# Optimization experiments

Hardware: AMD Instinct MI355X
Metric: run time of the kernel (lower is better)

## Reference

```python
import jax, jax.numpy as jnp
import numpy as np

N_NODES = 100000
N_EDGES = 3200000
D_IN = 16
D_OUT = 32


def setup_inputs() -> dict:
    key = jax.random.key(0)
    ks = jax.random.split(key, 8)
    x = jax.random.normal(ks[0], (N_NODES, D_IN), dtype=jnp.float32)
    edge_index = jax.random.randint(ks[1], (2, N_EDGES), 0, N_NODES, dtype=jnp.int64)
    s = 1.0 / np.sqrt(D_IN)
    # mlp1: Linear(16,16) -> ReLU -> Linear(16,16)
    w1 = jax.random.uniform(ks[2], (D_IN, D_IN), jnp.float32, -s, s)
    b1 = jax.random.uniform(ks[3], (D_IN,), jnp.float32, -s, s)
    w2 = jax.random.uniform(ks[4], (D_IN, D_IN), jnp.float32, -s, s)
    b2 = jax.random.uniform(ks[5], (D_IN,), jnp.float32, -s, s)
    # SAGEConv(16,32): lin_l (neighbors, with bias), lin_r (root, no bias)
    wl = jax.random.uniform(ks[6], (D_IN, D_OUT), jnp.float32, -s, s)
    bl = jnp.zeros((D_OUT,), jnp.float32)
    wr = jax.random.uniform(ks[7], (D_IN, D_OUT), jnp.float32, -s, s)
    return {"x": x, "edge_index": edge_index, "w1": w1, "b1": b1,
            "w2": w2, "b2": b2, "wl": wl, "bl": bl, "wr": wr}


def reference(x, edge_index, w1, b1, w2, b2, wl, bl, wr):
    # MLP: Linear -> ReLU -> Linear
    h = jax.nn.relu(x @ w1 + b1) @ w2 + b2  # [N, 16]
    src, dst = edge_index[0], edge_index[1]
    # mean aggregation of neighbor (source) features at destination nodes
    msg = h[src]  # [E, 16]
    summed = jax.ops.segment_sum(msg, dst, num_segments=N_NODES)  # [N, 16]
    cnt = jax.ops.segment_sum(jnp.ones((msg.shape[0],), h.dtype), dst,
                              num_segments=N_NODES)
    mean = summed / jnp.maximum(cnt, 1.0)[:, None]
    # SAGEConv: lin_l(aggr) + lin_r(root)
    out = mean @ wl + bl + h @ wr  # [N, 32]
    return out
```

## Files before the change

kernel.cpp:

```cpp
#include <hip/hip_runtime.h>
#include <hip/hip_bf16.h>

#define D_IN_C 16
#define BUCKET_SHIFT 9
#define BUCKET_NODES 512
#define CAP 18432
#define PT 16
#define PART_CHUNK 4096

__global__ __launch_bounds__(256) void mlp_kernel(
    const float* __restrict__ x,
    const float* __restrict__ w1, const float* __restrict__ b1,
    const float* __restrict__ w2, const float* __restrict__ b2,
    float* __restrict__ h, int* __restrict__ bcur,
    int n_nodes) {
  __shared__ float sw1[256];
  __shared__ float sw2[256];
  __shared__ float sb1[16];
  __shared__ float sb2[16];
  int t = threadIdx.x;
  if (blockIdx.x == 0) bcur[t] = 0;
  sw1[t] = w1[t];
  sw2[t] = w2[t];
  if (t < 16) { sb1[t] = b1[t]; sb2[t] = b2[t]; }
  __syncthreads();

  int n = blockIdx.x * blockDim.x + t;
  if (n >= n_nodes) return;

  float xi[16];
  const float4* xr = (const float4*)(x + (size_t)n * 16);
  float4 v0 = xr[0], v1 = xr[1], v2 = xr[2], v3 = xr[3];
  xi[0]=v0.x; xi[1]=v0.y; xi[2]=v0.z; xi[3]=v0.w;
  xi[4]=v1.x; xi[5]=v1.y; xi[6]=v1.z; xi[7]=v1.w;
  xi[8]=v2.x; xi[9]=v2.y; xi[10]=v2.z; xi[11]=v2.w;
  xi[12]=v3.x; xi[13]=v3.y; xi[14]=v3.z; xi[15]=v3.w;

  float t1[16];
#pragma unroll
  for (int j = 0; j < 16; ++j) {
    float acc = sb1[j];
#pragma unroll
    for (int k = 0; k < 16; ++k) acc += xi[k] * sw1[k * 16 + j];
    t1[j] = fmaxf(acc, 0.0f);
  }
  float hh[16];
#pragma unroll
  for (int j = 0; j < 16; ++j) {
    float acc = sb2[j];
#pragma unroll
    for (int k = 0; k < 16; ++k) acc += t1[k] * sw2[k * 16 + j];
    hh[j] = acc;
  }

  float4* hw = (float4*)(h + (size_t)n * 16);
  hw[0] = make_float4(hh[0], hh[1], hh[2], hh[3]);
  hw[1] = make_float4(hh[4], hh[5], hh[6], hh[7]);
  hw[2] = make_float4(hh[8], hh[9], hh[10], hh[11]);
  hw[3] = make_float4(hh[12], hh[13], hh[14], hh[15]);
}

__global__ __launch_bounds__(256) void part_kernel(
    const int* __restrict__ src, const int* __restrict__ dst,
    int* __restrict__ bcur, int* __restrict__ part,
    int* __restrict__ cnt, int nbuck, int n_edges) {
  __shared__ int lhist[256];
  __shared__ int lofs[256];
  int t = threadIdx.x;
  int base = blockIdx.x * PART_CHUNK;

  int zi = blockIdx.x * 256 + t;
  if (zi < nbuck * BUCKET_NODES) cnt[zi] = 0;

  if (t < nbuck) lhist[t] = 0;
  __syncthreads();

  int d[PT], s[PT];
#pragma unroll
  for (int i = 0; i < PT; ++i) {
    int e = base + i * 256 + t;
    if (e < n_edges) { d[i] = dst[e]; s[i] = src[e]; }
    else d[i] = -1;
  }
#pragma unroll
  for (int i = 0; i < PT; ++i) {
    if (d[i] >= 0) atomicAdd(&lhist[d[i] >> BUCKET_SHIFT], 1);
  }
  __syncthreads();
  if (t < nbuck) {
    int c = lhist[t];
    int r = (c > 0) ? atomicAdd(&bcur[t], c) : 0;
    lofs[t] = t * CAP + r;
  }
  __syncthreads();
#pragma unroll
  for (int i = 0; i < PT; ++i) {
    if (d[i] >= 0) {
      int b = d[i] >> BUCKET_SHIFT;
      int p = atomicAdd(&lofs[b], 1);
      part[p] = ((d[i] & (BUCKET_NODES - 1)) << 17) | s[i];
    }
  }
}

__global__ __launch_bounds__(256) void acc_kernel(
    const float* __restrict__ h, const int* __restrict__ part,
    const int* __restrict__ bcur, int* __restrict__ cnt,
    float* __restrict__ partial,
    int nbuck, int C) {
  __shared__ float acc[BUCKET_NODES * 16];
  __shared__ int dcnt[BUCKET_NODES];
  int t = threadIdx.x;
  int b = blockIdx.x / C;
  int c = blockIdx.x % C;

#pragma unroll
  for (int i = t; i < BUCKET_NODES * 16; i += 256) acc[i] = 0.0f;
  if (t < 256) { dcnt[t] = 0; dcnt[t + 256] = 0; }
  __syncthreads();

  int count = bcur[b];
  int start = b * CAP + (int)((long long)count * c / C);
  int end   = b * CAP + (int)((long long)count * (c + 1) / C);

  int g = t >> 4;
  int k = t & 15;

  for (int it = start; it < end; it += 128) {
    int pk[8]; float v[8];
#pragma unroll
    for (int u = 0; u < 8; ++u) {
      int e = it + u * 16 + g;
      pk[u] = (e < end) ? part[e] : -1;
    }
#pragma unroll
    for (int u = 0; u < 8; ++u) {
      v[u] = (pk[u] >= 0) ? h[(size_t)(pk[u] & 0x1FFFF) * 16 + k] : 0.0f;
    }
#pragma unroll
    for (int u = 0; u < 8; ++u) {
      if (pk[u] >= 0) {
        int dl = pk[u] >> 17;
        atomicAdd(&acc[dl * 16 + k], v[u]);
        if (k == 0) atomicAdd(&dcnt[dl], 1);
      }
    }
  }
  __syncthreads();

  float* pout = partial + (size_t)c * nbuck * BUCKET_NODES * 16
                        + (size_t)b * BUCKET_NODES * 16;
#pragma unroll
  for (int i = t; i < BUCKET_NODES * 16; i += 256) pout[i] = acc[i];
  if (t < 256) {
    int n0 = b * BUCKET_NODES + t;
    int n1 = n0 + 256;
    if (dcnt[t]) atomicAdd(&cnt[n0], dcnt[t]);
    if (dcnt[t + 256]) atomicAdd(&cnt[n1], dcnt[t + 256]);
  }
}

__global__ __launch_bounds__(256) void out_kernel(
    const float* __restrict__ h, const float* __restrict__ partial,
    const int* __restrict__ cnt,
    const float* __restrict__ wl, const float* __restrict__ bl,
    const float* __restrict__ wr, float* __restrict__ out,
    int n_nodes, int nbuck, int C) {
  __shared__ float swl[512];
  __shared__ float swr[512];
  __shared__ float sbl[32];
  int t = threadIdx.x;
  for (int i = t; i < 512; i += 256) { swl[i] = wl[i]; swr[i] = wr[i]; }
  if (t < 32) sbl[t] = bl[t];
  __syncthreads();

  int n = blockIdx.x * 256 + t;
  if (n >= n_nodes) return;

  size_t stride = (size_t)nbuck * BUCKET_NODES * 16;
  float mean[16];
#pragma unroll
  for (int k = 0; k < 16; ++k) mean[k] = 0.0f;
  for (int c = 0; c < C; ++c) {
    const float4* pr = (const float4*)(partial + c * stride + (size_t)n * 16);
    float4 p0 = pr[0], p1 = pr[1], p2 = pr[2], p3 = pr[3];
    mean[0]+=p0.x; mean[1]+=p0.y; mean[2]+=p0.z; mean[3]+=p0.w;
    mean[4]+=p1.x; mean[5]+=p1.y; mean[6]+=p1.z; mean[7]+=p1.w;
    mean[8]+=p2.x; mean[9]+=p2.y; mean[10]+=p2.z; mean[11]+=p2.w;
    mean[12]+=p3.x; mean[13]+=p3.y; mean[14]+=p3.z; mean[15]+=p3.w;
  }
  float inv = 1.0f / fmaxf((float)cnt[n], 1.0f);
#pragma unroll
  for (int k = 0; k < 16; ++k) mean[k] *= inv;

  float hr[16];
  const float4* hp = (const float4*)(h + (size_t)n * 16);
  float4 h0 = hp[0], h1 = hp[1], h2 = hp[2], h3 = hp[3];
  hr[0]=h0.x; hr[1]=h0.y; hr[2]=h0.z; hr[3]=h0.w;
  hr[4]=h1.x; hr[5]=h1.y; hr[6]=h1.z; hr[7]=h1.w;
  hr[8]=h2.x; hr[9]=h2.y; hr[10]=h2.z; hr[11]=h2.w;
  hr[12]=h3.x; hr[13]=h3.y; hr[14]=h3.z; hr[15]=h3.w;

  float o[32];
#pragma unroll
  for (int j = 0; j < 32; ++j) o[j] = sbl[j];
#pragma unroll
  for (int k = 0; k < 16; ++k) {
#pragma unroll
    for (int j = 0; j < 32; ++j) {
      o[j] += mean[k] * swl[k * 32 + j] + hr[k] * swr[k * 32 + j];
    }
  }
  float4* ow = (float4*)(out + (size_t)n * 32);
#pragma unroll
  for (int q = 0; q < 8; ++q)
    ow[q] = make_float4(o[q*4], o[q*4+1], o[q*4+2], o[q*4+3]);
}

extern "C" void kernel_launch(void* const* d_in, const int* in_sizes, int n_in,
                              void* d_out, int out_size, void* d_ws, size_t ws_size,
                              hipStream_t stream) {
  const float* x  = (const float*)d_in[0];
  const int* eidx = (const int*)d_in[1];
  const float* w1 = (const float*)d_in[2];
  const float* b1 = (const float*)d_in[3];
  const float* w2 = (const float*)d_in[4];
  const float* b2 = (const float*)d_in[5];
  const float* wl = (const float*)d_in[6];
  const float* bl = (const float*)d_in[7];
  const float* wr = (const float*)d_in[8];
  float* out = (float*)d_out;

  const int n_nodes = in_sizes[0] / D_IN_C;
  const int n_edges = in_sizes[1] / 2;
  const int* src = eidx;
  const int* dst = eidx + n_edges;

  const int nbuck = (n_nodes + BUCKET_NODES - 1) / BUCKET_NODES;

  float* h     = (float*)d_ws;
  int* part    = (int*)(h + (size_t)n_nodes * 16);
  int* bcur    = part + (size_t)nbuck * CAP;
  int* cnt     = bcur + 256;
  float* partial = (float*)(cnt + (size_t)nbuck * BUCKET_NODES);

  size_t fixed = (size_t)n_nodes * 16 * 4 + (size_t)nbuck * CAP * 4
               + 256 * 4 + (size_t)nbuck * BUCKET_NODES * 4;
  size_t per_copy = (size_t)nbuck * BUCKET_NODES * 16 * 4;
  int C = (ws_size >= fixed + 4 * per_copy) ? 4 : 2;

  mlp_kernel<<<(n_nodes + 255) / 256, 256, 0, stream>>>(
      x, w1, b1, w2, b2, h, bcur, n_nodes);
  part_kernel<<<(n_edges + PART_CHUNK - 1) / PART_CHUNK, 256, 0, stream>>>(
      src, dst, bcur, part, cnt, nbuck, n_edges);
  acc_kernel<<<nbuck * C, 256, 0, stream>>>(
      h, part, bcur, cnt, partial, nbuck, C);
  out_kernel<<<(n_nodes + 255) / 256, 256, 0, stream>>>(
      h, partial, cnt, wl, bl, wr, out, n_nodes, nbuck, C);
}
```

Measured before the change: 479.5 us.

## Widen accumulate blocks to 512 threads, split buckets more, drop bounds checks

The edge-accumulation kernel now runs 512 threads per block, so each iteration handles 32 edges. The main loop runs full 256-edge tiles without per-element bounds checks, and a separate loop handles the remainder. The partial write-out uses float4 stores, and up to 8 partial copies per bucket are allowed when workspace permits. This spreads the gather and atomic work over more blocks and waves. The cost is that the output kernel must reduce more partial copies and the larger block uses more registers.

```diff
diff --git a/kernel.cpp b/kernel.cpp
--- a/kernel.cpp
+++ b/kernel.cpp
@@ -103,7 +103,7 @@
   }
 }
 
-__global__ __launch_bounds__(256) void acc_kernel(
+__global__ __launch_bounds__(512, 6) void acc_kernel(
     const float* __restrict__ h, const int* __restrict__ part,
     const int* __restrict__ bcur, int* __restrict__ cnt,
     float* __restrict__ partial,
@@ -115,8 +115,8 @@
   int c = blockIdx.x % C;
 
 #pragma unroll
-  for (int i = t; i < BUCKET_NODES * 16; i += 256) acc[i] = 0.0f;
-  if (t < 256) { dcnt[t] = 0; dcnt[t + 256] = 0; }
+  for (int i = t; i < BUCKET_NODES * 16; i += 512) acc[i] = 0.0f;
+  dcnt[t] = 0;
   __syncthreads();
 
   int count = bcur[b];
@@ -126,38 +126,40 @@
   int g = t >> 4;
   int k = t & 15;
 
-  for (int it = start; it < end; it += 128) {
-    int pk[8]; float v[8];
+  int nfull = (end - start) >> 8;
+  int e = start;
+  for (int f = 0; f < nfull; ++f, e += 256) {
+    int pk[8];
+#pragma unroll
+    for (int u = 0; u < 8; ++u) pk[u] = part[e + u * 32 + g];
+    float v[8];
+#pragma unroll
+    for (int u = 0; u < 8; ++u)
+      v[u] = h[((unsigned)(pk[u] & 0x1FFFF) << 4) | (unsigned)k];
 #pragma unroll
     for (int u = 0; u < 8; ++u) {
-      int e = it + u * 16 + g;
-      pk[u] = (e < end) ? part[e] : -1;
+      unsigned dl = (unsigned)pk[u] >> 17;
+      atomicAdd(&acc[(dl << 4) | (unsigned)k], v[u]);
+      if (k == 0) atomicAdd(&dcnt[dl], 1);
     }
-#pragma unroll
-    for (int u = 0; u < 8; ++u) {
-      v[u] = (pk[u] >= 0) ? h[(size_t)(pk[u] & 0x1FFFF) * 16 + k] : 0.0f;
-    }
-#pragma unroll
-    for (int u = 0; u < 8; ++u) {
-      if (pk[u] >= 0) {
-        int dl = pk[u] >> 17;
-        atomicAdd(&acc[dl * 16 + k], v[u]);
-        if (k == 0) atomicAdd(&dcnt[dl], 1);
-      }
-    }
+  }
+  for (int ee = e + g; ee < end; ee += 32) {
+    int pk = part[ee];
+    float v = h[((unsigned)(pk & 0x1FFFF) << 4) | (unsigned)k];
+    unsigned dl = (unsigned)pk >> 17;
+    atomicAdd(&acc[(dl << 4) | (unsigned)k], v);
+    if (k == 0) atomicAdd(&dcnt[dl], 1);
   }
   __syncthreads();
 
   float* pout = partial + (size_t)c * nbuck * BUCKET_NODES * 16
                         + (size_t)b * BUCKET_NODES * 16;
-#pragma unroll
-  for (int i = t; i < BUCKET_NODES * 16; i += 256) pout[i] = acc[i];
-  if (t < 256) {
-    int n0 = b * BUCKET_NODES + t;
-    int n1 = n0 + 256;
-    if (dcnt[t]) atomicAdd(&cnt[n0], dcnt[t]);
-    if (dcnt[t + 256]) atomicAdd(&cnt[n1], dcnt[t + 256]);
-  }
+  float4* pout4 = (float4*)pout;
+  const float4* a4 = (const float4*)acc;
+#pragma unroll
+  for (int i = t; i < BUCKET_NODES * 4; i += 512) pout4[i] = a4[i];
+  int dc = dcnt[t];
+  if (dc) atomicAdd(&cnt[b * BUCKET_NODES + t], dc);
 }
 
 __global__ __launch_bounds__(256) void out_kernel(
@@ -247,13 +249,15 @@
   size_t fixed = (size_t)n_nodes * 16 * 4 + (size_t)nbuck * CAP * 4
                + 256 * 4 + (size_t)nbuck * BUCKET_NODES * 4;
   size_t per_copy = (size_t)nbuck * BUCKET_NODES * 16 * 4;
-  int C = (ws_size >= fixed + 4 * per_copy) ? 4 : 2;
+  int C = 2;
+  if (ws_size >= fixed + 8 * per_copy) C = 8;
+  else if (ws_size >= fixed + 4 * per_copy) C = 4;
 
   mlp_kernel<<<(n_nodes + 255) / 256, 256, 0, stream>>>(
       x, w1, b1, w2, b2, h, bcur, n_nodes);
   part_kernel<<<(n_edges + PART_CHUNK - 1) / PART_CHUNK, 256, 0, stream>>>(
       src, dst, bcur, part, cnt, nbuck, n_edges);
-  acc_kernel<<<nbuck * C, 256, 0, stream>>>(
+  acc_kernel<<<nbuck * C, 512, 0, stream>>>(
       h, part, bcur, cnt, partial, nbuck, C);
   out_kernel<<<(n_nodes + 255) / 256, 256, 0, stream>>>(
       h, partial, cnt, wl, bl, wr, out, n_nodes, nbuck, C);
```

Result: faster. 444.2 us (-7.4%).
